# Performance work log

Hardware: AMD Instinct MI355X
Metric: run time of the kernel (lower is better)

Reference implementation:

```python
import jax, jax.numpy as jnp
import numpy as np
from jax import lax

IMG_SIZE = 512        # efficientdet-d0 input resolution
TOP_K = 256           # fixed candidate count for jit-compatible NMS
THRESHOLD = 0.01      # score threshold (init kwarg)
IOU_THRESHOLD = 0.5   # NMS IoU threshold (init kwarg)


def make_anchors():
    """Standard EfficientDet-d0 anchors: P3-P7, 3 scales x 3 ratios, xyxy."""
    strides = [8, 16, 32, 64, 128]
    scales = [2.0 ** 0, 2.0 ** (1.0 / 3.0), 2.0 ** (2.0 / 3.0)]
    ratios = [0.5, 1.0, 2.0]
    base = 4.0
    out = []
    for s in strides:
        fs = IMG_SIZE // s
        xs = (np.arange(fs, dtype=np.float32) + 0.5) * s
        cy, cx = np.meshgrid(xs, xs, indexing='ij')
        for r in ratios:
            for sc in scales:
                w = base * s * sc * np.sqrt(1.0 / r)
                h = base * s * sc * np.sqrt(r)
                a = np.stack([cx - w / 2, cy - h / 2, cx + w / 2, cy + h / 2], -1)
                out.append(a.reshape(-1, 4))
    return np.concatenate(out, 0).astype(np.float32)  # [49104, 4]


def decode_boxes(anchors, regs):
    """RetinaNet-style delta decode. anchors [A,4] xyxy, regs [B,A,4]."""
    aw = anchors[:, 2] - anchors[:, 0]
    ah = anchors[:, 3] - anchors[:, 1]
    acx = anchors[:, 0] + 0.5 * aw
    acy = anchors[:, 1] + 0.5 * ah
    dx, dy, dw, dh = regs[..., 0], regs[..., 1], regs[..., 2], regs[..., 3]
    cx = acx + dx * aw
    cy = acy + dy * ah
    w = aw * jnp.exp(jnp.clip(dw, -4.0, 4.0))
    h = ah * jnp.exp(jnp.clip(dh, -4.0, 4.0))
    boxes = jnp.stack([cx - 0.5 * w, cy - 0.5 * h, cx + 0.5 * w, cy + 0.5 * h], -1)
    return jnp.clip(boxes, 0.0, float(IMG_SIZE))  # [B,A,4]


def pairwise_iou(boxes):
    """boxes [K,4] xyxy -> iou [K,K]."""
    area = jnp.maximum(boxes[:, 2] - boxes[:, 0], 0) * jnp.maximum(boxes[:, 3] - boxes[:, 1], 0)
    lt = jnp.maximum(boxes[:, None, :2], boxes[None, :, :2])
    rb = jnp.minimum(boxes[:, None, 2:], boxes[None, :, 2:])
    wh = jnp.maximum(rb - lt, 0.0)
    inter = wh[..., 0] * wh[..., 1]
    union = area[:, None] + area[None, :] - inter
    return inter / jnp.maximum(union, 1e-8)


def nms_keep(boxes, scores):
    """Sequential NMS over score-sorted candidates. boxes [K,4], scores [K]."""
    K = boxes.shape[0]
    iou = pairwise_iou(boxes)  # [K,K]
    ar = jnp.arange(K)
    keep0 = scores > 0.0

    def body(i, keep):
        suppressed = jnp.any(keep & (iou[:, i] > IOU_THRESHOLD) & (ar < i))
        return keep.at[i].set(keep[i] & ~suppressed)

    return lax.fori_loop(0, K, body, keep0)


def setup_inputs() -> dict:
    key = jax.random.key(0)
    k1, k2 = jax.random.split(key)
    B, A, C = 8, 49104, 80
    cls_logits = jax.random.normal(k1, (B, A, C), dtype=jnp.float32) - 2.0
    box_regs = 0.2 * jax.random.normal(k2, (B, A, 4), dtype=jnp.float32)
    anchors = jnp.asarray(make_anchors())
    return {"cls_logits": cls_logits, "box_regs": box_regs, "anchors": anchors}


def reference(cls_logits, box_regs, anchors):
    probs = jax.nn.sigmoid(cls_logits)            # [B,A,C]
    scores = probs.max(-1)                        # [B,A]
    labels = probs.argmax(-1)                     # [B,A]
    boxes = decode_boxes(anchors, box_regs)       # [B,A,4]
    scores = jnp.where(scores > THRESHOLD, scores, 0.0)
    top_s, idx = lax.top_k(scores, TOP_K)         # [B,K]
    top_b = jnp.take_along_axis(boxes, idx[..., None], axis=1)   # [B,K,4]
    top_l = jnp.take_along_axis(labels, idx, axis=1)             # [B,K]
    keep = jax.vmap(nms_keep)(top_b, top_s)                      # [B,K] bool
    keep_f = keep.astype(top_b.dtype)
    dets = jnp.concatenate([top_b * keep_f[..., None], (top_s * keep_f)[..., None]], -1)  # [B,K,5]
    return dets, top_l, keep
```

## Files before the change

kernel.cpp:

```cpp
#include <hip/hip_runtime.h>
#include <hip/hip_cooperative_groups.h>
#include <stdint.h>
#include <math.h>

namespace cg = cooperative_groups;

#define IMGF   512.0f
#define A_N    49104
#define B_N    8
#define C_N    80
#define K_N    256
#define IOU_T  0.5f
#define NBIN   4096
#define CAP    2048
#define GRID_N 256
#define TOTAL_A (B_N * A_N)

__device__ __forceinline__ int bin_of(uint32_t key) {
    float s = __uint_as_float(key);
    int b = (int)(s * 4096.0f);
    return b > 4095 ? 4095 : b;
}

__global__ __launch_bounds__(1024) void fused_kernel(
    const float* __restrict__ logits,
    const float* __restrict__ regs,
    const float* __restrict__ anchors,
    uint32_t* __restrict__ keys,
    float* __restrict__ out)
{
    const int tid  = threadIdx.x;
    const int lane = tid & 63, wv = tid >> 6;
    const int grp  = lane >> 2, j = lane & 3;

    for (int g = blockIdx.x * 256 + wv * 16 + grp; g < TOTAL_A; g += GRID_N * 256) {
        const float4* p = (const float4*)(logits + (size_t)g * C_N);
        float4 v0 = p[j], v1 = p[j + 4], v2 = p[j + 8], v3 = p[j + 12], v4 = p[j + 16];
        float m = fmaxf(fmaxf(fmaxf(v0.x, v0.y), fmaxf(v0.z, v0.w)),
                        fmaxf(fmaxf(v1.x, v1.y), fmaxf(v1.z, v1.w)));
        m = fmaxf(m, fmaxf(fmaxf(v2.x, v2.y), fmaxf(v2.z, v2.w)));
        m = fmaxf(m, fmaxf(fmaxf(v3.x, v3.y), fmaxf(v3.z, v3.w)));
        m = fmaxf(m, fmaxf(fmaxf(v4.x, v4.y), fmaxf(v4.z, v4.w)));
        m = fmaxf(m, __shfl_xor(m, 1, 64));
        m = fmaxf(m, __shfl_xor(m, 2, 64));
        if (j == 0) {
            float s = 1.0f / (1.0f + expf(-m));
            if (!(s > 0.01f)) s = 0.0f;
            keys[g] = __float_as_uint(s);
        }
    }

    cg::this_grid().sync();

    if (blockIdx.x >= B_N) return;
    const int b = blockIdx.x;

    __shared__ uint32_t hist[NBIN];
    __shared__ int wtots[16];
    __shared__ int sh_T, sh_nc;
    __shared__ unsigned long long cand[CAP];
    __shared__ unsigned long long sorted[K_N];
    __shared__ float4 sbox[K_N];
    __shared__ float  sscore[K_N];
    __shared__ int    slab[K_N];
    __shared__ unsigned long long supr[K_N][4];
    __shared__ unsigned long long keepw[4];

    const uint32_t* kb = keys + (size_t)b * A_N;
    const uint4* kb4 = (const uint4*)kb;
    const int N4 = A_N / 4;

    for (int i = tid; i < NBIN; i += 1024) hist[i] = 0;
    if (tid == 0) sh_nc = 0;
    __syncthreads();
    for (int i = tid; i < N4; i += 1024) {
        uint4 v = kb4[i];
        atomicAdd(&hist[bin_of(v.x)], 1u);
        atomicAdd(&hist[bin_of(v.y)], 1u);
        atomicAdd(&hist[bin_of(v.z)], 1u);
        atomicAdd(&hist[bin_of(v.w)], 1u);
    }
    __syncthreads();

    const int lo = tid * 4;
    int seg = (int)hist[lo] + (int)hist[lo + 1]
            + (int)hist[lo + 2] + (int)hist[lo + 3];
    int s1 = seg;
#pragma unroll
    for (int off = 1; off < 64; off <<= 1) {
        int v = __shfl_down(s1, off, 64);
        if (lane + off < 64) s1 += v;
    }
    if (lane == 0) wtots[wv] = s1;
    __syncthreads();
    int wsuf = 0;
    for (int w = wv + 1; w < 16; ++w) wsuf += wtots[w];
    int above = wsuf + (s1 - seg);
    if (above < K_N && above + seg >= K_N) {
        int cum = above;
        for (int bin = lo + 3; bin >= lo; --bin) {
            int c = (int)hist[bin];
            if (cum + c >= K_N) { sh_T = bin; break; }
            cum += c;
        }
    }
    __syncthreads();
    const int T = sh_T;

    for (int i = tid; i < N4; i += 1024) {
        uint4 v = kb4[i];
        uint32_t ks[4] = { v.x, v.y, v.z, v.w };
#pragma unroll
        for (int q = 0; q < 4; ++q) {
            if (bin_of(ks[q]) >= T) {
                int p = atomicAdd(&sh_nc, 1);
                if (p < CAP)
                    cand[p] = ((unsigned long long)ks[q] << 32)
                            | (unsigned long long)(0xFFFFFFFFu - (uint32_t)(4 * i + q));
            }
        }
    }
    if (tid < K_N) sorted[tid] = 0ull;
    __syncthreads();
    int nc = sh_nc; if (nc > CAP) nc = CAP;

    for (int i = tid; i < nc; i += 1024) {
        unsigned long long me = cand[i];
        int r = 0;
        for (int jq = 0; jq < nc; ++jq) r += (cand[jq] > me);
        if (r < K_N) sorted[r] = me;
    }
    __syncthreads();

    if (tid < K_N) {
#pragma clang fp contract(off)
        unsigned long long cv = sorted[tid];
        uint32_t key = (uint32_t)(cv >> 32);
        uint32_t ai  = 0xFFFFFFFFu - (uint32_t)cv;
        if (ai >= (uint32_t)A_N) ai = 0;
        int a = (int)ai;
        float s = __uint_as_float(key);
        sscore[tid] = s;

        {
            const float4* lp = (const float4*)(logits + ((size_t)b * A_N + a) * C_N);
            float best = -INFINITY; int cls = 0;
#pragma unroll
            for (int k = 0; k < 20; ++k) {
                float4 w = lp[k];
                if (w.x > best) { best = w.x; cls = 4 * k + 0; }
                if (w.y > best) { best = w.y; cls = 4 * k + 1; }
                if (w.z > best) { best = w.z; cls = 4 * k + 2; }
                if (w.w > best) { best = w.w; cls = 4 * k + 3; }
            }
            slab[tid] = cls;
        }

        float ax0 = anchors[4 * a + 0], ay0 = anchors[4 * a + 1];
        float ax1 = anchors[4 * a + 2], ay1 = anchors[4 * a + 3];
        float aw = ax1 - ax0, ah = ay1 - ay0;
        float acx = ax0 + 0.5f * aw, acy = ay0 + 0.5f * ah;
        const float* r = regs + ((size_t)b * A_N + a) * 4;
        float dx = r[0], dy = r[1], dw = r[2], dh = r[3];
        float cx = acx + dx * aw;
        float cy = acy + dy * ah;
        dw = fminf(fmaxf(dw, -4.0f), 4.0f);
        dh = fminf(fmaxf(dh, -4.0f), 4.0f);
        float w = aw * expf(dw);
        float h = ah * expf(dh);
        float x0 = cx - 0.5f * w, y0 = cy - 0.5f * h;
        float x1 = cx + 0.5f * w, y1 = cy + 0.5f * h;
        x0 = fminf(fmaxf(x0, 0.0f), IMGF);
        y0 = fminf(fmaxf(y0, 0.0f), IMGF);
        x1 = fminf(fmaxf(x1, 0.0f), IMGF);
        y1 = fminf(fmaxf(y1, 0.0f), IMGF);
        sbox[tid] = make_float4(x0, y0, x1, y1);
    }
    __syncthreads();

    {
#pragma clang fp contract(off)
        const int row = tid & 255, gq = tid >> 8;
        float4 bi = sbox[row];
        float areai = fmaxf(bi.z - bi.x, 0.0f) * fmaxf(bi.w - bi.y, 0.0f);
        unsigned long long m = 0;
        const int jlo = gq * 64, jhi = jlo + 64;
        int start = row + 1 > jlo ? row + 1 : jlo;
        for (int jx = start; jx < jhi; ++jx) {
            float4 bj = sbox[jx];
            float areaj = fmaxf(bj.z - bj.x, 0.0f) * fmaxf(bj.w - bj.y, 0.0f);
            float lx = fmaxf(bi.x, bj.x), ly = fmaxf(bi.y, bj.y);
            float rx = fminf(bi.z, bj.z), ry = fminf(bi.w, bj.w);
            float iw = fmaxf(rx - lx, 0.0f), ih = fmaxf(ry - ly, 0.0f);
            float inter = iw * ih;
            float uni = areai + areaj - inter;
            float iou = inter / fmaxf(uni, 1e-8f);
            if (iou > IOU_T) m |= 1ull << (jx & 63);
        }
        supr[row][gq] = m;
    }
    if (tid < K_N) {
        unsigned long long ball = __ballot(sscore[tid] > 0.0f);
        if ((tid & 63) == 0) keepw[tid >> 6] = ball;
    }
    __syncthreads();

    if (tid == 0) {
        unsigned long long k0 = keepw[0], k1 = keepw[1], k2 = keepw[2], k3 = keepw[3];
#define NMS_CHUNK(c, kc)                                                     \
        for (int l = 0; l < 64; ++l) {                                       \
            const int i = (c) * 64 + l;                                      \
            unsigned long long w0 = supr[i][0], w1 = supr[i][1];             \
            unsigned long long w2 = supr[i][2], w3 = supr[i][3];             \
            if ((kc >> l) & 1ull) {                                          \
                k0 &= ~w0; k1 &= ~w1; k2 &= ~w2; k3 &= ~w3;                  \
            }                                                                \
        }
        NMS_CHUNK(0, k0)
        NMS_CHUNK(1, k1)
        NMS_CHUNK(2, k2)
        NMS_CHUNK(3, k3)
#undef NMS_CHUNK
        keepw[0] = k0; keepw[1] = k1; keepw[2] = k2; keepw[3] = k3;
    }
    __syncthreads();

    if (tid < K_N) {
        float keepf = ((keepw[tid >> 6] >> (tid & 63)) & 1ull) ? 1.0f : 0.0f;
        float4 bx = sbox[tid];
        float s = sscore[tid];
        float* det = out + ((size_t)b * K_N + tid) * 5;
        det[0] = bx.x * keepf;
        det[1] = bx.y * keepf;
        det[2] = bx.z * keepf;
        det[3] = bx.w * keepf;
        det[4] = s * keepf;
        out[(size_t)B_N * K_N * 5 + (size_t)b * K_N + tid] = (float)slab[tid];
        out[(size_t)B_N * K_N * 5 + (size_t)B_N * K_N + (size_t)b * K_N + tid] = keepf;
    }
}

extern "C" void kernel_launch(void* const* d_in, const int* in_sizes, int n_in,
                              void* d_out, int out_size, void* d_ws, size_t ws_size,
                              hipStream_t stream)
{
    const float* logits  = (const float*)d_in[0];
    const float* regs    = (const float*)d_in[1];
    const float* anchors = (const float*)d_in[2];
    float* out = (float*)d_out;

    uint32_t* keys = (uint32_t*)d_ws;

    void* args[] = { (void*)&logits, (void*)&regs, (void*)&anchors,
                     (void*)&keys, (void*)&out };
    hipLaunchCooperativeKernel((const void*)fused_kernel,
                               dim3(GRID_N), dim3(1024), args, 0, stream);
}
```

Baseline: 282.9 us.

## Double-buffer logit loads, compute labels in pass one, pick grid by occupancy

The first pass now double-buffers the per-anchor logit loads across grid-stride iterations so the next row's loads are in flight while the current row is reduced. The same pass computes the argmax class with a tie-break and stores it as a byte label, which removes the second read of 80 logits per top-k candidate. The grid is chosen at runtime (512 or 256 blocks) from an occupancy query, and the serial NMS loop is unrolled by four. The costs are more registers under the tighter launch bounds, one extra byte written per anchor, and a workspace that must be large enough to hold the labels after the keys.

```diff
diff --git a/kernel.cpp b/kernel.cpp
--- a/kernel.cpp
+++ b/kernel.cpp
@@ -13,7 +13,6 @@
 #define IOU_T  0.5f
 #define NBIN   4096
 #define CAP    2048
-#define GRID_N 256
 #define TOTAL_A (B_N * A_N)
 
 __device__ __forceinline__ int bin_of(uint32_t key) {
@@ -22,32 +21,67 @@
     return b > 4095 ? 4095 : b;
 }
 
-__global__ __launch_bounds__(1024) void fused_kernel(
+__device__ __forceinline__ void amax4(float4 v, int cbase, float& best, int& cls) {
+    if (v.x > best) { best = v.x; cls = cbase + 0; }
+    if (v.y > best) { best = v.y; cls = cbase + 1; }
+    if (v.z > best) { best = v.z; cls = cbase + 2; }
+    if (v.w > best) { best = v.w; cls = cbase + 3; }
+}
+
+template <int GRID>
+__global__ __launch_bounds__(1024, 8) void fused_kernel(
     const float* __restrict__ logits,
     const float* __restrict__ regs,
     const float* __restrict__ anchors,
     uint32_t* __restrict__ keys,
+    uint8_t* __restrict__ labels,
     float* __restrict__ out)
 {
     const int tid  = threadIdx.x;
     const int lane = tid & 63, wv = tid >> 6;
     const int grp  = lane >> 2, j = lane & 3;
-
-    for (int g = blockIdx.x * 256 + wv * 16 + grp; g < TOTAL_A; g += GRID_N * 256) {
-        const float4* p = (const float4*)(logits + (size_t)g * C_N);
-        float4 v0 = p[j], v1 = p[j + 4], v2 = p[j + 8], v3 = p[j + 12], v4 = p[j + 16];
-        float m = fmaxf(fmaxf(fmaxf(v0.x, v0.y), fmaxf(v0.z, v0.w)),
-                        fmaxf(fmaxf(v1.x, v1.y), fmaxf(v1.z, v1.w)));
-        m = fmaxf(m, fmaxf(fmaxf(v2.x, v2.y), fmaxf(v2.z, v2.w)));
-        m = fmaxf(m, fmaxf(fmaxf(v3.x, v3.y), fmaxf(v3.z, v3.w)));
-        m = fmaxf(m, fmaxf(fmaxf(v4.x, v4.y), fmaxf(v4.z, v4.w)));
-        m = fmaxf(m, __shfl_xor(m, 1, 64));
-        m = fmaxf(m, __shfl_xor(m, 2, 64));
-        if (j == 0) {
-            float s = 1.0f / (1.0f + expf(-m));
-            if (!(s > 0.01f)) s = 0.0f;
-            keys[g] = __float_as_uint(s);
-        }
+    const int STR  = GRID * 256;
+
+    {
+        float4 A0, A1, A2, A3, A4, B0, B1, B2, B3, B4;
+#define LOAD5(R, g) { const float4* p = (const float4*)(logits + (size_t)(g) * C_N); \
+        R##0 = p[j]; R##1 = p[j + 4]; R##2 = p[j + 8]; R##3 = p[j + 12]; R##4 = p[j + 16]; }
+#define RED_STORE(R, g) { \
+        float best = -INFINITY; int cls = 0; \
+        amax4(R##0,      4 * j, best, cls); \
+        amax4(R##1, 16 + 4 * j, best, cls); \
+        amax4(R##2, 32 + 4 * j, best, cls); \
+        amax4(R##3, 48 + 4 * j, best, cls); \
+        amax4(R##4, 64 + 4 * j, best, cls); \
+        { float mo = __shfl_xor(best, 1, 64); int co = __shfl_xor(cls, 1, 64); \
+          if (mo > best || (mo == best && co < cls)) { best = mo; cls = co; } } \
+        { float mo = __shfl_xor(best, 2, 64); int co = __shfl_xor(cls, 2, 64); \
+          if (mo > best || (mo == best && co < cls)) { best = mo; cls = co; } } \
+        if (j == 0) { \
+            float s = 1.0f / (1.0f + expf(-best)); \
+            if (!(s > 0.01f)) s = 0.0f; \
+            keys[g] = __float_as_uint(s); \
+            labels[g] = (uint8_t)cls; \
+        } }
+
+        int g = blockIdx.x * 256 + wv * 16 + grp;
+        LOAD5(A, g);
+        while (true) {
+            int gn = g + STR;
+            bool has = gn < TOTAL_A;
+            if (has) { LOAD5(B, gn); }
+            RED_STORE(A, g);
+            if (!has) break;
+            g = gn;
+            int gm = g + STR;
+            bool has2 = gm < TOTAL_A;
+            if (has2) { LOAD5(A, gm); }
+            RED_STORE(B, g);
+            if (!has2) break;
+            g = gm;
+        }
+#undef LOAD5
+#undef RED_STORE
     }
 
     cg::this_grid().sync();
@@ -141,20 +175,7 @@
         int a = (int)ai;
         float s = __uint_as_float(key);
         sscore[tid] = s;
-
-        {
-            const float4* lp = (const float4*)(logits + ((size_t)b * A_N + a) * C_N);
-            float best = -INFINITY; int cls = 0;
-#pragma unroll
-            for (int k = 0; k < 20; ++k) {
-                float4 w = lp[k];
-                if (w.x > best) { best = w.x; cls = 4 * k + 0; }
-                if (w.y > best) { best = w.y; cls = 4 * k + 1; }
-                if (w.z > best) { best = w.z; cls = 4 * k + 2; }
-                if (w.w > best) { best = w.w; cls = 4 * k + 3; }
-            }
-            slab[tid] = cls;
-        }
+        slab[tid] = (int)labels[(size_t)b * A_N + a];
 
         float ax0 = anchors[4 * a + 0], ay0 = anchors[4 * a + 1];
         float ax1 = anchors[4 * a + 2], ay1 = anchors[4 * a + 3];
@@ -207,14 +228,21 @@
 
     if (tid == 0) {
         unsigned long long k0 = keepw[0], k1 = keepw[1], k2 = keepw[2], k3 = keepw[3];
-#define NMS_CHUNK(c, kc)                                                     \
-        for (int l = 0; l < 64; ++l) {                                       \
-            const int i = (c) * 64 + l;                                      \
-            unsigned long long w0 = supr[i][0], w1 = supr[i][1];             \
-            unsigned long long w2 = supr[i][2], w3 = supr[i][3];             \
-            if ((kc >> l) & 1ull) {                                          \
-                k0 &= ~w0; k1 &= ~w1; k2 &= ~w2; k3 &= ~w3;                  \
-            }                                                                \
+#define NMS_CHUNK(c, kc)                                                       \
+        for (int l = 0; l < 64; l += 4) {                                      \
+            const int i = (c) * 64 + l;                                        \
+            unsigned long long wA0 = supr[i+0][0], wA1 = supr[i+0][1],         \
+                               wA2 = supr[i+0][2], wA3 = supr[i+0][3];         \
+            unsigned long long wB0 = supr[i+1][0], wB1 = supr[i+1][1],         \
+                               wB2 = supr[i+1][2], wB3 = supr[i+1][3];         \
+            unsigned long long wC0 = supr[i+2][0], wC1 = supr[i+2][1],         \
+                               wC2 = supr[i+2][2], wC3 = supr[i+2][3];         \
+            unsigned long long wD0 = supr[i+3][0], wD1 = supr[i+3][1],         \
+                               wD2 = supr[i+3][2], wD3 = supr[i+3][3];         \
+            if ((kc >> (l + 0)) & 1ull) { k0 &= ~wA0; k1 &= ~wA1; k2 &= ~wA2; k3 &= ~wA3; } \
+            if ((kc >> (l + 1)) & 1ull) { k0 &= ~wB0; k1 &= ~wB1; k2 &= ~wB2; k3 &= ~wB3; } \
+            if ((kc >> (l + 2)) & 1ull) { k0 &= ~wC0; k1 &= ~wC1; k2 &= ~wC2; k3 &= ~wC3; } \
+            if ((kc >> (l + 3)) & 1ull) { k0 &= ~wD0; k1 &= ~wD1; k2 &= ~wD2; k3 &= ~wD3; } \
         }
         NMS_CHUNK(0, k0)
         NMS_CHUNK(1, k1)
@@ -249,10 +277,24 @@
     const float* anchors = (const float*)d_in[2];
     float* out = (float*)d_out;
 
-    uint32_t* keys = (uint32_t*)d_ws;
+    uint32_t* keys   = (uint32_t*)d_ws;
+    uint8_t*  labels = (uint8_t*)(keys + (size_t)B_N * A_N);
 
     void* args[] = { (void*)&logits, (void*)&regs, (void*)&anchors,
-                     (void*)&keys, (void*)&out };
-    hipLaunchCooperativeKernel((const void*)fused_kernel,
-                               dim3(GRID_N), dim3(1024), args, 0, stream);
+                     (void*)&keys, (void*)&labels, (void*)&out };
+
+    static int grid_choice = -1;
+    if (grid_choice < 0) {
+        int nb = 0;
+        hipError_t e = hipOccupancyMaxActiveBlocksPerMultiprocessor(
+            &nb, fused_kernel<512>, 1024, 0);
+        grid_choice = (e == hipSuccess && nb >= 2) ? 512 : 256;
+    }
+    if (grid_choice == 512) {
+        hipLaunchCooperativeKernel(fused_kernel<512>, dim3(512), dim3(1024),
+                                   args, 0, stream);
+    } else {
+        hipLaunchCooperativeKernel(fused_kernel<256>, dim3(256), dim3(1024),
+                                   args, 0, stream);
+    }
 }
```

Result: no change. 286.7 us (+1.3%).
